# Kernel tuning notes

Hardware: AMD Instinct MI355X
Metric: run time of the kernel (lower is better)

## Reference

```python
import jax, jax.numpy as jnp
import numpy as np

DIM = 256
WS = 7          # window_size
NH = 8          # num_heads
HD = DIM // NH  # head_dim = 32
SCALE = HD ** (-0.5)
B = 4096        # batch * num_windows
N = WS * WS     # 49 tokens per window


def _rel_pos_index(ws):
    coords = np.stack(np.meshgrid(np.arange(ws), np.arange(ws), indexing='ij'))
    cf = coords.transpose(1, 2, 0).reshape(-1, 2)                 # [N,2]
    rel = cf[:, None, :] - cf[None, :, :]                          # [N,N,2]
    rel[:, :, 0] += ws - 1
    rel[:, :, 1] += ws - 1
    rel[:, :, 0] *= 2 * ws - 1
    return jnp.asarray(rel.sum(-1).astype(np.int32))               # [N,N]

REL_IDX = _rel_pos_index(WS)


def setup_inputs() -> dict:
    key = jax.random.key(0)
    ks = jax.random.split(key, 8)
    x = jax.random.normal(ks[0], (B, N, DIM), dtype=jnp.float32)
    mask = jax.random.normal(ks[1], (B, 1, N, N), dtype=jnp.float32)
    qkv_w = jax.random.normal(ks[2], (DIM, 3 * DIM), dtype=jnp.float32) * 0.02
    qkv_b = jnp.zeros((3 * DIM,), dtype=jnp.float32)
    rpb_table = jax.random.normal(ks[3], ((2 * WS - 1) ** 2, NH), dtype=jnp.float32) * 0.02
    proj_w = jax.random.normal(ks[4], (DIM, DIM), dtype=jnp.float32) * 0.02
    proj_b = jnp.zeros((DIM,), dtype=jnp.float32)
    return {"x": x, "mask": mask, "qkv_w": qkv_w, "qkv_b": qkv_b,
            "rpb_table": rpb_table, "proj_w": proj_w, "proj_b": proj_b}


def reference(x, mask, qkv_w, qkv_b, rpb_table, proj_w, proj_b):
    b, n, c = x.shape
    qkv = x @ qkv_w + qkv_b                                        # [b,n,3c]
    qkv = qkv.reshape(b, n, 3, NH, HD).transpose(2, 0, 3, 1, 4)    # [3,b,h,n,d]
    q, k, v = qkv[0], qkv[1], qkv[2]
    attn = jnp.einsum('bhnd,bhmd->bhnm', q * SCALE, k)             # [b,h,n,n]
    bias = rpb_table[REL_IDX.reshape(-1)].reshape(n, n, NH)        # [n,n,h]
    attn = attn + bias.transpose(2, 0, 1)[None] + mask             # [b,h,n,n]
    attn = jax.nn.softmax(attn, axis=-1)
    out = jnp.einsum('bhnm,bhmd->bhnd', attn, v)                   # [b,h,n,d]
    out = out.transpose(0, 2, 1, 3).reshape(b, n, c)               # [b,n,c]
    return out @ proj_w + proj_b
```

## Files before the change

### kernel.cpp

```cpp
#include <hip/hip_runtime.h>
#include <cstdint>
#include <cstddef>


#define NTOK 49
#define SCALE 0.17677669529663687f

typedef unsigned short u16;
typedef __attribute__((ext_vector_type(8))) short short8;
typedef __attribute__((ext_vector_type(4))) float f32x4;

__device__ __forceinline__ u16 f2bf(float f) {
    unsigned int u = __float_as_uint(f);
    u = (u + 0x7FFFu + ((u >> 16) & 1u)) >> 16;
    return (u16)u;
}

__global__ void prep_weights(const float* __restrict__ qkv_w,
                             const float* __restrict__ proj_w,
                             u16* __restrict__ qkv_wT,
                             u16* __restrict__ proj_wT) {
    int i = blockIdx.x * 256 + threadIdx.x;
    if (i < 768 * 256) {
        int oc = i >> 8, k = i & 255;
        qkv_wT[i] = f2bf(qkv_w[k * 768 + oc]);
    }
    int j = i - 768 * 256;
    if (j >= 0 && j < 256 * 256) {
        int oc = j >> 8, k = j & 255;
        proj_wT[j] = f2bf(proj_w[k * 256 + oc]);
    }
}

__global__ __launch_bounds__(256) void qkv_gemm(
        const float* __restrict__ x, const u16* __restrict__ wT,
        const float* __restrict__ bias, u16* __restrict__ qkv) {
    __shared__ __align__(16) u16 As[128][72];
    __shared__ __align__(16) u16 Bs[128][72];
    const int bid = blockIdx.x;
    const int m0 = (bid / 6) * 128, n0 = (bid % 6) * 128;
    const int t = threadIdx.x;
    const int lane = t & 63, w = t >> 6;
    const int quad = lane >> 4, l16 = lane & 15;
    const int wm = w >> 1, wn = w & 1;
    f32x4 acc[4][4] = {};
    for (int kk = 0; kk < 256; kk += 64) {
        {
            const int c4 = t & 15, rg = t >> 4;
            #pragma unroll
            for (int i = 0; i < 8; ++i) {
                const int row = rg + i * 16;
                const f32x4 v = *(const f32x4*)(x + (size_t)(m0 + row) * 256 + kk + c4 * 4);
                ushort4 pk;
                pk.x = f2bf(v.x); pk.y = f2bf(v.y); pk.z = f2bf(v.z); pk.w = f2bf(v.w);
                *(ushort4*)&As[row][c4 * 4] = pk;
            }
        }
        {
            const int c8 = t & 7, rg = t >> 3;
            #pragma unroll
            for (int i = 0; i < 4; ++i) {
                const int row = rg + i * 32;
                *(uint4*)&Bs[row][c8 * 8] =
                    *(const uint4*)(wT + (size_t)(n0 + row) * 256 + kk + c8 * 8);
            }
        }
        __syncthreads();
        #pragma unroll
        for (int ks = 0; ks < 2; ++ks) {
            short8 af[4], bfr[4];
            #pragma unroll
            for (int i = 0; i < 4; ++i)
                af[i] = *(const short8*)&As[wm * 64 + i * 16 + l16][ks * 32 + quad * 8];
            #pragma unroll
            for (int j = 0; j < 4; ++j)
                bfr[j] = *(const short8*)&Bs[wn * 64 + j * 16 + l16][ks * 32 + quad * 8];
            #pragma unroll
            for (int i = 0; i < 4; ++i)
                #pragma unroll
                for (int j = 0; j < 4; ++j)
                    acc[i][j] = __builtin_amdgcn_mfma_f32_16x16x32_bf16(
                        af[i], bfr[j], acc[i][j], 0, 0, 0);
        }
        __syncthreads();
    }
    #pragma unroll
    for (int j = 0; j < 4; ++j) {
        const int gc = n0 + wn * 64 + j * 16 + l16;
        const float bv = bias[gc];
        const float scl = (gc < 256) ? SCALE : 1.0f;
        #pragma unroll
        for (int i = 0; i < 4; ++i) {
            const int gr = m0 + wm * 64 + i * 16 + quad * 4;
            #pragma unroll
            for (int r = 0; r < 4; ++r)
                qkv[(size_t)(gr + r) * 768 + gc] = f2bf((acc[i][j][r] + bv) * scl);
        }
    }
}

__global__ __launch_bounds__(512) void attn_proj(
        const u16* __restrict__ qkv, const float* __restrict__ mask,
        const float* __restrict__ rpb, const u16* __restrict__ projT,
        const float* __restrict__ proj_b, float* __restrict__ out) {
    __shared__ __align__(16) u16 QKs[49][520];
    __shared__ __align__(16) u16 Vt[8][32 * 72];
    __shared__ __align__(16) u16 Ps[8][16][72];
    __shared__ __align__(16) u16 OutS[49][264];
    const int b = blockIdx.x;
    const int t = threadIdx.x;
    const int lane = t & 63, h = t >> 6;
    const int quad = lane >> 4, l16 = lane & 15;
    const short8 zf = {0, 0, 0, 0, 0, 0, 0, 0};
    const f32x4 zero4 = {0.f, 0.f, 0.f, 0.f};

    {
        unsigned int* vz = (unsigned int*)&Vt[0][0];
        for (int i = t; i < 8 * 32 * 72 / 2; i += 512) vz[i] = 0;
    }
    __syncthreads();
    const u16* qrow = qkv + (size_t)b * NTOK * 768;
    for (int ch = t; ch < 49 * 64; ch += 512) {
        const int n = ch >> 6, c8 = ch & 63;
        *(uint4*)&QKs[n][c8 * 8] = *(const uint4*)(qrow + n * 768 + c8 * 8);
    }
    for (int e = t; e < 49 * 256; e += 512) {
        const int n = e >> 8, hd = e & 255;
        Vt[hd >> 5][(hd & 31) * 72 + n] = qrow[n * 768 + 512 + hd];
    }
    __syncthreads();

    short8 aQ[4], bK[4];
    #pragma unroll
    for (int i = 0; i < 4; ++i) {
        const int r = i * 16 + l16;
        aQ[i] = (r < 49) ? *(const short8*)&QKs[r][h * 32 + quad * 8] : zf;
        bK[i] = (r < 49) ? *(const short8*)&QKs[r][256 + h * 32 + quad * 8] : zf;
    }
    f32x4 S[4][4];
    #pragma unroll
    for (int i = 0; i < 4; ++i)
        #pragma unroll
        for (int j = 0; j < 4; ++j)
            S[i][j] = __builtin_amdgcn_mfma_f32_16x16x32_bf16(aQ[i], bK[j], zero4, 0, 0, 0);

    const float* mrow = mask + (size_t)b * (NTOK * NTOK);
    int c7[4], cm[4], cc[4];
    #pragma unroll
    for (int j = 0; j < 4; ++j) {
        cc[j] = j * 16 + l16;
        c7[j] = (cc[j] * 37) >> 8;
        cm[j] = cc[j] - c7[j] * 7;
    }
    #pragma unroll
    for (int i = 0; i < 4; ++i) {
        #pragma unroll
        for (int r = 0; r < 4; ++r) {
            const int row = i * 16 + quad * 4 + r;
            const int r7 = (row * 37) >> 8;
            const int rm = row - r7 * 7;
            #pragma unroll
            for (int j = 0; j < 4; ++j) {
                float s = -1e30f;
                if (row < 49 && cc[j] < 49) {
                    const int idx = (r7 - c7[j] + 6) * 13 + (rm - cm[j] + 6);
                    s = S[i][j][r] + rpb[idx * 8 + h] + mrow[row * 49 + cc[j]];
                }
                S[i][j][r] = s;
            }
            float mx = fmaxf(fmaxf(S[i][0][r], S[i][1][r]),
                             fmaxf(S[i][2][r], S[i][3][r]));
            #pragma unroll
            for (int off = 1; off < 16; off <<= 1) mx = fmaxf(mx, __shfl_xor(mx, off));
            float sum = 0.f;
            #pragma unroll
            for (int j = 0; j < 4; ++j) {
                const float e = __expf(S[i][j][r] - mx);
                S[i][j][r] = e;
                sum += e;
            }
            #pragma unroll
            for (int off = 1; off < 16; off <<= 1) sum += __shfl_xor(sum, off);
            const float rinv = 1.0f / sum;
            #pragma unroll
            for (int j = 0; j < 4; ++j) S[i][j][r] = S[i][j][r] * rinv;
        }
    }

    short8 bV[2][2];
    #pragma unroll
    for (int ct = 0; ct < 2; ++ct)
        #pragma unroll
        for (int ks = 0; ks < 2; ++ks)
            bV[ct][ks] = *(const short8*)&Vt[h][(ct * 16 + l16) * 72 + ks * 32 + quad * 8];
    f32x4 O[4][2] = {};
    #pragma unroll
    for (int i = 0; i < 4; ++i) {
        __threadfence_block();
        #pragma unroll
        for (int j = 0; j < 4; ++j)
            #pragma unroll
            for (int r = 0; r < 4; ++r)
                Ps[h][quad * 4 + r][j * 16 + l16] = f2bf(S[i][j][r]);
        __threadfence_block();
        const short8 aP0 = *(const short8*)&Ps[h][l16][quad * 8];
        const short8 aP1 = *(const short8*)&Ps[h][l16][32 + quad * 8];
        #pragma unroll
        for (int ct = 0; ct < 2; ++ct) {
            O[i][ct] = __builtin_amdgcn_mfma_f32_16x16x32_bf16(aP0, bV[ct][0], O[i][ct], 0, 0, 0);
            O[i][ct] = __builtin_amdgcn_mfma_f32_16x16x32_bf16(aP1, bV[ct][1], O[i][ct], 0, 0, 0);
        }
    }
    #pragma unroll
    for (int i = 0; i < 4; ++i)
        #pragma unroll
        for (int ct = 0; ct < 2; ++ct)
            #pragma unroll
            for (int r = 0; r < 4; ++r) {
                const int row = i * 16 + quad * 4 + r;
                if (row < 49) OutS[row][h * 32 + ct * 16 + l16] = f2bf(O[i][ct][r]);
            }
    __syncthreads();

    f32x4 P2[4][2] = {};
    #pragma unroll
    for (int ks = 0; ks < 8; ++ks) {
        short8 bW[2];
        #pragma unroll
        for (int ct = 0; ct < 2; ++ct)
            bW[ct] = *(const short8*)(projT + (size_t)(h * 32 + ct * 16 + l16) * 256
                                      + ks * 32 + quad * 8);
        #pragma unroll
        for (int i = 0; i < 4; ++i) {
            const int row = i * 16 + l16;
            const short8 aO = (row < 49) ? *(const short8*)&OutS[row][ks * 32 + quad * 8] : zf;
            #pragma unroll
            for (int ct = 0; ct < 2; ++ct)
                P2[i][ct] = __builtin_amdgcn_mfma_f32_16x16x32_bf16(aO, bW[ct], P2[i][ct], 0, 0, 0);
        }
    }
    #pragma unroll
    for (int ct = 0; ct < 2; ++ct) {
        const int gc = h * 32 + ct * 16 + l16;
        const float pb = proj_b[gc];
        #pragma unroll
        for (int i = 0; i < 4; ++i)
            #pragma unroll
            for (int r = 0; r < 4; ++r) {
                const int row = i * 16 + quad * 4 + r;
                if (row < 49)
                    out[((size_t)b * NTOK + row) * 256 + gc] = P2[i][ct][r] + pb;
            }
    }
}

extern "C" void kernel_launch(void* const* d_in, const int* in_sizes, int n_in,
                              void* d_out, int out_size, void* d_ws, size_t ws_size,
                              hipStream_t stream) {
    const float* x      = (const float*)d_in[0];
    const float* mask   = (const float*)d_in[1];
    const float* qkv_w  = (const float*)d_in[2];
    const float* qkv_b  = (const float*)d_in[3];
    const float* rpb    = (const float*)d_in[4];
    const float* proj_w = (const float*)d_in[5];
    const float* proj_b = (const float*)d_in[6];
    float* outp = (float*)d_out;

    u16* qkv     = (u16*)d_ws;
    u16* qkv_wT  = qkv + (size_t)200704 * 768;
    u16* proj_wT = qkv_wT + 768 * 256;

    prep_weights<<<1024, 256, 0, stream>>>(qkv_w, proj_w, qkv_wT, proj_wT);
    qkv_gemm<<<1568 * 6, 256, 0, stream>>>(x, qkv_wT, qkv_b, qkv);
    attn_proj<<<4096, 512, 0, stream>>>(qkv, mask, rpb, proj_wT, proj_b, outp);
}
```

Baseline: 964.6 us.

## Widen QKV GEMM tiles with async LDS loads and slim attention LDS usage

The QKV GEMM now uses 512-thread blocks computing 128x256 tiles, loads weight tiles straight into LDS via global_load_lds, and orders blocks so consecutive blocks share the same weight columns. The attention kernel drops the Q/K staging buffer, reading Q and K fragments directly from global memory. It also reuses the V-transpose buffer as the softmax P scratch and processes one row tile at a time to cut LDS and register pressure. Together these aim to reduce LDS footprint and raise occupancy (launch bounds set to 4 blocks). The trade-offs are unpadded GEMM LDS rows that may cause bank conflicts, and uncoalesced direct global reads for Q/K.

```diff
diff --git a/kernel.cpp b/kernel.cpp
--- a/kernel.cpp
+++ b/kernel.cpp
@@ -14,6 +14,12 @@
     unsigned int u = __float_as_uint(f);
     u = (u + 0x7FFFu + ((u >> 16) & 1u)) >> 16;
     return (u16)u;
+}
+
+__device__ __forceinline__ void async_lds16(void* lds, const void* g) {
+    __builtin_amdgcn_global_load_lds(
+        (const __attribute__((address_space(1))) void*)g,
+        (__attribute__((address_space(3))) void*)lds, 16, 0, 0);
 }
 
 __global__ void prep_weights(const float* __restrict__ qkv_w,
@@ -32,38 +38,43 @@
     }
 }
 
-__global__ __launch_bounds__(256) void qkv_gemm(
+__global__ __launch_bounds__(512, 4) void qkv_gemm(
         const float* __restrict__ x, const u16* __restrict__ wT,
         const float* __restrict__ bias, u16* __restrict__ qkv) {
-    __shared__ __align__(16) u16 As[128][72];
-    __shared__ __align__(16) u16 Bs[128][72];
+    __shared__ __align__(16) u16 As[128 * 64];
+    __shared__ __align__(16) u16 Bs[256 * 64];
     const int bid = blockIdx.x;
-    const int m0 = (bid / 6) * 128, n0 = (bid % 6) * 128;
+    const int m0 = (bid % 1568) * 128, n0 = (bid / 1568) * 256;
     const int t = threadIdx.x;
     const int lane = t & 63, w = t >> 6;
     const int quad = lane >> 4, l16 = lane & 15;
-    const int wm = w >> 1, wn = w & 1;
+    const int wm = w & 1, wn = w >> 1;
+    const int ar = t >> 2, ac = (t & 3) * 16;
+    const int br = t >> 3, bc = (t & 7) * 8;
     f32x4 acc[4][4] = {};
     for (int kk = 0; kk < 256; kk += 64) {
+        #pragma unroll
+        for (int c = 0; c < 4; ++c)
+            async_lds16(&Bs[c * 4096 + t * 8],
+                        wT + (size_t)(n0 + c * 64 + br) * 256 + kk + bc);
         {
-            const int c4 = t & 15, rg = t >> 4;
-            #pragma unroll
-            for (int i = 0; i < 8; ++i) {
-                const int row = rg + i * 16;
-                const f32x4 v = *(const f32x4*)(x + (size_t)(m0 + row) * 256 + kk + c4 * 4);
-                ushort4 pk;
-                pk.x = f2bf(v.x); pk.y = f2bf(v.y); pk.z = f2bf(v.z); pk.w = f2bf(v.w);
-                *(ushort4*)&As[row][c4 * 4] = pk;
-            }
-        }
-        {
-            const int c8 = t & 7, rg = t >> 3;
-            #pragma unroll
-            for (int i = 0; i < 4; ++i) {
-                const int row = rg + i * 32;
-                *(uint4*)&Bs[row][c8 * 8] =
-                    *(const uint4*)(wT + (size_t)(n0 + row) * 256 + kk + c8 * 8);
-            }
+            const float* src = x + (size_t)(m0 + ar) * 256 + kk + ac;
+            const f32x4 v0 = *(const f32x4*)(src);
+            const f32x4 v1 = *(const f32x4*)(src + 4);
+            const f32x4 v2 = *(const f32x4*)(src + 8);
+            const f32x4 v3 = *(const f32x4*)(src + 12);
+            ushort4 p0, p1, p2, p3;
+            p0.x=f2bf(v0.x); p0.y=f2bf(v0.y); p0.z=f2bf(v0.z); p0.w=f2bf(v0.w);
+            p1.x=f2bf(v1.x); p1.y=f2bf(v1.y); p1.z=f2bf(v1.z); p1.w=f2bf(v1.w);
+            p2.x=f2bf(v2.x); p2.y=f2bf(v2.y); p2.z=f2bf(v2.z); p2.w=f2bf(v2.w);
+            p3.x=f2bf(v3.x); p3.y=f2bf(v3.y); p3.z=f2bf(v3.z); p3.w=f2bf(v3.w);
+            uint4 q0, q1;
+            q0.x=*(unsigned*)&p0.x; q0.y=*(unsigned*)&p0.z;
+            q0.z=*(unsigned*)&p1.x; q0.w=*(unsigned*)&p1.z;
+            q1.x=*(unsigned*)&p2.x; q1.y=*(unsigned*)&p2.z;
+            q1.z=*(unsigned*)&p3.x; q1.w=*(unsigned*)&p3.z;
+            *(uint4*)&As[ar * 64 + ac] = q0;
+            *(uint4*)&As[ar * 64 + ac + 8] = q1;
         }
         __syncthreads();
         #pragma unroll
@@ -71,10 +82,10 @@
             short8 af[4], bfr[4];
             #pragma unroll
             for (int i = 0; i < 4; ++i)
-                af[i] = *(const short8*)&As[wm * 64 + i * 16 + l16][ks * 32 + quad * 8];
+                af[i] = *(const short8*)&As[(wm * 64 + i * 16 + l16) * 64 + ks * 32 + quad * 8];
             #pragma unroll
             for (int j = 0; j < 4; ++j)
-                bfr[j] = *(const short8*)&Bs[wn * 64 + j * 16 + l16][ks * 32 + quad * 8];
+                bfr[j] = *(const short8*)&Bs[(wn * 64 + j * 16 + l16) * 64 + ks * 32 + quad * 8];
             #pragma unroll
             for (int i = 0; i < 4; ++i)
                 #pragma unroll
@@ -99,13 +110,11 @@
     }
 }
 
-__global__ __launch_bounds__(512) void attn_proj(
+__global__ __launch_bounds__(512, 4) void attn_proj(
         const u16* __restrict__ qkv, const float* __restrict__ mask,
         const float* __restrict__ rpb, const u16* __restrict__ projT,
         const float* __restrict__ proj_b, float* __restrict__ out) {
-    __shared__ __align__(16) u16 QKs[49][520];
-    __shared__ __align__(16) u16 Vt[8][32 * 72];
-    __shared__ __align__(16) u16 Ps[8][16][72];
+    __shared__ __align__(16) u16 Vt[8][32 * 68];
     __shared__ __align__(16) u16 OutS[49][264];
     const int b = blockIdx.x;
     const int t = threadIdx.x;
@@ -116,44 +125,55 @@
 
     {
         unsigned int* vz = (unsigned int*)&Vt[0][0];
-        for (int i = t; i < 8 * 32 * 72 / 2; i += 512) vz[i] = 0;
+        for (int i = t; i < 8 * 32 * 68 / 2; i += 512) vz[i] = 0;
     }
     __syncthreads();
     const u16* qrow = qkv + (size_t)b * NTOK * 768;
-    for (int ch = t; ch < 49 * 64; ch += 512) {
-        const int n = ch >> 6, c8 = ch & 63;
-        *(uint4*)&QKs[n][c8 * 8] = *(const uint4*)(qrow + n * 768 + c8 * 8);
-    }
-    for (int e = t; e < 49 * 256; e += 512) {
-        const int n = e >> 8, hd = e & 255;
-        Vt[hd >> 5][(hd & 31) * 72 + n] = qrow[n * 768 + 512 + hd];
+    for (int idx = t; idx < NTOK * 64; idx += 512) {
+        const int n = idx >> 6, hd = (idx & 63) * 4;
+        const ushort4 v = *(const ushort4*)(qrow + n * 768 + 512 + hd);
+        u16* vt = &Vt[hd >> 5][0];
+        const int d = hd & 31;
+        vt[(d + 0) * 68 + n] = v.x;
+        vt[(d + 1) * 68 + n] = v.y;
+        vt[(d + 2) * 68 + n] = v.z;
+        vt[(d + 3) * 68 + n] = v.w;
     }
     __syncthreads();
 
-    short8 aQ[4], bK[4];
-    #pragma unroll
-    for (int i = 0; i < 4; ++i) {
-        const int r = i * 16 + l16;
-        aQ[i] = (r < 49) ? *(const short8*)&QKs[r][h * 32 + quad * 8] : zf;
-        bK[i] = (r < 49) ? *(const short8*)&QKs[r][256 + h * 32 + quad * 8] : zf;
-    }
-    f32x4 S[4][4];
-    #pragma unroll
-    for (int i = 0; i < 4; ++i)
-        #pragma unroll
-        for (int j = 0; j < 4; ++j)
-            S[i][j] = __builtin_amdgcn_mfma_f32_16x16x32_bf16(aQ[i], bK[j], zero4, 0, 0, 0);
-
+    short8 bK[4];
+    #pragma unroll
+    for (int j = 0; j < 4; ++j) {
+        const int r = j * 16 + l16;
+        bK[j] = (r < NTOK) ? *(const short8*)(qrow + r * 768 + 256 + h * 32 + quad * 8) : zf;
+    }
+    short8 bV[2][2];
+    #pragma unroll
+    for (int ct = 0; ct < 2; ++ct)
+        #pragma unroll
+        for (int ks = 0; ks < 2; ++ks)
+            bV[ct][ks] = *(const short8*)&Vt[h][(ct * 16 + l16) * 68 + ks * 32 + quad * 8];
+    __threadfence_block();
+
+    u16* Ps = &Vt[h][0];
     const float* mrow = mask + (size_t)b * (NTOK * NTOK);
-    int c7[4], cm[4], cc[4];
+    int cc[4], c7[4], cm[4];
     #pragma unroll
     for (int j = 0; j < 4; ++j) {
         cc[j] = j * 16 + l16;
         c7[j] = (cc[j] * 37) >> 8;
         cm[j] = cc[j] - c7[j] * 7;
     }
+
     #pragma unroll
     for (int i = 0; i < 4; ++i) {
+        const int qr = i * 16 + l16;
+        const short8 aQ = (qr < NTOK)
+            ? *(const short8*)(qrow + qr * 768 + h * 32 + quad * 8) : zf;
+        f32x4 S[4];
+        #pragma unroll
+        for (int j = 0; j < 4; ++j)
+            S[j] = __builtin_amdgcn_mfma_f32_16x16x32_bf16(aQ, bK[j], zero4, 0, 0, 0);
         #pragma unroll
         for (int r = 0; r < 4; ++r) {
             const int row = i * 16 + quad * 4 + r;
@@ -162,64 +182,50 @@
             #pragma unroll
             for (int j = 0; j < 4; ++j) {
                 float s = -1e30f;
-                if (row < 49 && cc[j] < 49) {
+                if (row < NTOK && cc[j] < NTOK) {
                     const int idx = (r7 - c7[j] + 6) * 13 + (rm - cm[j] + 6);
-                    s = S[i][j][r] + rpb[idx * 8 + h] + mrow[row * 49 + cc[j]];
+                    s = S[j][r] + rpb[idx * 8 + h] + mrow[row * 49 + cc[j]];
                 }
-                S[i][j][r] = s;
-            }
-            float mx = fmaxf(fmaxf(S[i][0][r], S[i][1][r]),
-                             fmaxf(S[i][2][r], S[i][3][r]));
+                S[j][r] = s;
+            }
+            float mx = fmaxf(fmaxf(S[0][r], S[1][r]), fmaxf(S[2][r], S[3][r]));
             #pragma unroll
             for (int off = 1; off < 16; off <<= 1) mx = fmaxf(mx, __shfl_xor(mx, off));
             float sum = 0.f;
             #pragma unroll
             for (int j = 0; j < 4; ++j) {
-                const float e = __expf(S[i][j][r] - mx);
-                S[i][j][r] = e;
+                const float e = __expf(S[j][r] - mx);
+                S[j][r] = e;
                 sum += e;
             }
             #pragma unroll
             for (int off = 1; off < 16; off <<= 1) sum += __shfl_xor(sum, off);
             const float rinv = 1.0f / sum;
             #pragma unroll
-            for (int j = 0; j < 4; ++j) S[i][j][r] = S[i][j][r] * rinv;
-        }
-    }
-
-    short8 bV[2][2];
-    #pragma unroll
-    for (int ct = 0; ct < 2; ++ct)
-        #pragma unroll
-        for (int ks = 0; ks < 2; ++ks)
-            bV[ct][ks] = *(const short8*)&Vt[h][(ct * 16 + l16) * 72 + ks * 32 + quad * 8];
-    f32x4 O[4][2] = {};
-    #pragma unroll
-    for (int i = 0; i < 4; ++i) {
+            for (int j = 0; j < 4; ++j) S[j][r] = S[j][r] * rinv;
+        }
         __threadfence_block();
         #pragma unroll
         for (int j = 0; j < 4; ++j)
             #pragma unroll
             for (int r = 0; r < 4; ++r)
-                Ps[h][quad * 4 + r][j * 16 + l16] = f2bf(S[i][j][r]);
+                Ps[(quad * 4 + r) * 68 + j * 16 + l16] = f2bf(S[j][r]);
         __threadfence_block();
-        const short8 aP0 = *(const short8*)&Ps[h][l16][quad * 8];
-        const short8 aP1 = *(const short8*)&Ps[h][l16][32 + quad * 8];
-        #pragma unroll
-        for (int ct = 0; ct < 2; ++ct) {
-            O[i][ct] = __builtin_amdgcn_mfma_f32_16x16x32_bf16(aP0, bV[ct][0], O[i][ct], 0, 0, 0);
-            O[i][ct] = __builtin_amdgcn_mfma_f32_16x16x32_bf16(aP1, bV[ct][1], O[i][ct], 0, 0, 0);
-        }
-    }
-    #pragma unroll
-    for (int i = 0; i < 4; ++i)
-        #pragma unroll
-        for (int ct = 0; ct < 2; ++ct)
-            #pragma unroll
-            for (int r = 0; r < 4; ++r) {
-                const int row = i * 16 + quad * 4 + r;
-                if (row < 49) OutS[row][h * 32 + ct * 16 + l16] = f2bf(O[i][ct][r]);
-            }
+        const short8 aP0 = *(const short8*)&Ps[l16 * 68 + quad * 8];
+        const short8 aP1 = *(const short8*)&Ps[l16 * 68 + 32 + quad * 8];
+        f32x4 O0 = __builtin_amdgcn_mfma_f32_16x16x32_bf16(aP0, bV[0][0], zero4, 0, 0, 0);
+        O0 = __builtin_amdgcn_mfma_f32_16x16x32_bf16(aP1, bV[0][1], O0, 0, 0, 0);
+        f32x4 O1 = __builtin_amdgcn_mfma_f32_16x16x32_bf16(aP0, bV[1][0], zero4, 0, 0, 0);
+        O1 = __builtin_amdgcn_mfma_f32_16x16x32_bf16(aP1, bV[1][1], O1, 0, 0, 0);
+        #pragma unroll
+        for (int r = 0; r < 4; ++r) {
+            const int row = i * 16 + quad * 4 + r;
+            if (row < NTOK) {
+                OutS[row][h * 32 + l16] = f2bf(O0[r]);
+                OutS[row][h * 32 + 16 + l16] = f2bf(O1[r]);
+            }
+        }
+    }
     __syncthreads();
 
     f32x4 P2[4][2] = {};
@@ -233,7 +239,7 @@
         #pragma unroll
         for (int i = 0; i < 4; ++i) {
             const int row = i * 16 + l16;
-            const short8 aO = (row < 49) ? *(const short8*)&OutS[row][ks * 32 + quad * 8] : zf;
+            const short8 aO = (row < NTOK) ? *(const short8*)&OutS[row][ks * 32 + quad * 8] : zf;
             #pragma unroll
             for (int ct = 0; ct < 2; ++ct)
                 P2[i][ct] = __builtin_amdgcn_mfma_f32_16x16x32_bf16(aO, bW[ct], P2[i][ct], 0, 0, 0);
@@ -248,7 +254,7 @@
             #pragma unroll
             for (int r = 0; r < 4; ++r) {
                 const int row = i * 16 + quad * 4 + r;
-                if (row < 49)
+                if (row < NTOK)
                     out[((size_t)b * NTOK + row) * 256 + gc] = P2[i][ct][r] + pb;
             }
     }
@@ -271,6 +277,6 @@
     u16* proj_wT = qkv_wT + 768 * 256;
 
     prep_weights<<<1024, 256, 0, stream>>>(qkv_w, proj_w, qkv_wT, proj_wT);
-    qkv_gemm<<<1568 * 6, 256, 0, stream>>>(x, qkv_wT, qkv_b, qkv);
+    qkv_gemm<<<1568 * 3, 512, 0, stream>>>(x, qkv_wT, qkv_b, qkv);
     attn_proj<<<4096, 512, 0, stream>>>(qkv, mask, rpb, proj_wT, proj_b, outp);
 }
```

After: 830.0 us. 14.0% less time.
